# Kernel optimization log

Measured on AMD Instinct MI355X. Metric: run time of the kernel, lower is better.

Reference implementation:

```python
import jax, jax.numpy as jnp
import numpy as np

EPS = 1e-8

def setup_inputs() -> dict:
    key = jax.random.key(0)
    k1, k2 = jax.random.split(key)
    N, C, S = 2000000, 32, 8
    feats = jax.random.normal(k1, (N, C), dtype=jnp.float32)
    seg_ids = jnp.sort(jax.random.randint(k2, (N,), 0, S, dtype=jnp.int32))
    weight = jnp.ones((1, C), dtype=jnp.float32)
    bias = jnp.zeros((1, C), dtype=jnp.float32)
    return {"feats": feats, "seg_ids": seg_ids, "weight": weight, "bias": bias, "num_segments": S}

def reference(feats, seg_ids, weight, bias, num_segments):
    # Per-instance (segment) mean: GlobalPoolingForward with average=True
    counts = jax.ops.segment_sum(jnp.ones((feats.shape[0], 1), feats.dtype), seg_ids,
                                 num_segments=num_segments)  # [S,1]
    counts = jnp.maximum(counts, 1.0)
    mean = jax.ops.segment_sum(feats, seg_ids, num_segments=num_segments) / counts  # [S,C]
    # BroadcastForward ADDITION with -mean
    centered = feats - mean[seg_ids]  # [N,C]
    # Second global pooling: per-instance variance
    var = jax.ops.segment_sum(centered * centered, seg_ids, num_segments=num_segments) / counts  # [S,C]
    inv_std = jax.lax.rsqrt(var + EPS)  # [S,C]
    # BroadcastForward MULTIPLICATION with inv_std, then affine
    norm = centered * inv_std[seg_ids]
    return norm * weight + bias
```

## Files before the change

### kernel.cpp

```cpp
#include <hip/hip_runtime.h>
#include <math.h>


#define WS_SUM   0
#define WS_SUMSQ 2048
#define WS_CNT   4096
#define WS_SCALE 4352
#define WS_SHIFT 6400

typedef float f32x4 __attribute__((ext_vector_type(4)));

__global__ void zero_ws_kernel(float* __restrict__ ws) {
    int t = blockIdx.x * blockDim.x + threadIdx.x;
    if (t < 4352) ws[t] = 0.0f;
}

#define ACC4(A, Q, V)                                        \
    do {                                                     \
        (A).x += (V).x; (A).y += (V).y;                      \
        (A).z += (V).z; (A).w += (V).w;                      \
        (Q).x += (V).x * (V).x; (Q).y += (V).y * (V).y;      \
        (Q).z += (V).z * (V).z; (Q).w += (V).w * (V).w;      \
    } while (0)

#define ADD4(A, B)                                           \
    do {                                                     \
        (A).x += (B).x; (A).y += (B).y;                      \
        (A).z += (B).z; (A).w += (B).w;                      \
    } while (0)

__global__ __launch_bounds__(256) void reduce_kernel(
        const float4* __restrict__ feats4, const int* __restrict__ seg,
        float* __restrict__ ws, int N, int chunk) {
    __shared__ float4 s_sum[256];
    __shared__ float4 s_sq[256];
    __shared__ int    s_c[256];
    float* sum_g   = ws + WS_SUM;
    float* sumsq_g = ws + WS_SUMSQ;
    float* cnt_g   = ws + WS_CNT;

    int t  = threadIdx.x;
    int cg = t & 7;
    int rl = t >> 3;
    int bstart = blockIdx.x * chunk;
    if (bstart >= N) return;
    int bend = min(N, bstart + chunk);
    int rows = bend - bstart;

    int seg_first = seg[bstart];
    int seg_last  = seg[bend - 1];

    if (seg_first == seg_last) {
        float4 a0 = make_float4(0.f,0.f,0.f,0.f), a1 = a0, a2 = a0, a3 = a0;
        float4 q0 = a0, q1 = a0, q2 = a0, q3 = a0;
        const float4* p = feats4 + (size_t)(bstart + rl) * 8 + cg;
        int r = rl;
        for (; r + 224 < rows; r += 256) {
            float4 v0 = p[0 * 256];
            float4 v1 = p[1 * 256];
            float4 v2 = p[2 * 256];
            float4 v3 = p[3 * 256];
            float4 v4 = p[4 * 256];
            float4 v5 = p[5 * 256];
            float4 v6 = p[6 * 256];
            float4 v7 = p[7 * 256];
            ACC4(a0, q0, v0);
            ACC4(a1, q1, v1);
            ACC4(a2, q2, v2);
            ACC4(a3, q3, v3);
            ACC4(a0, q0, v4);
            ACC4(a1, q1, v5);
            ACC4(a2, q2, v6);
            ACC4(a3, q3, v7);
            p += 8 * 256;
        }
        for (; r < rows; r += 32) {
            float4 v = *p;
            ACC4(a0, q0, v);
            p += 256;
        }
        ADD4(a0, a1); ADD4(a2, a3); ADD4(a0, a2);
        ADD4(q0, q1); ADD4(q2, q3); ADD4(q0, q2);
        s_sum[t] = a0;
        s_sq[t]  = q0;
        __syncthreads();
        for (int off = 128; off >= 8; off >>= 1) {
            if (t < off) {
                float4 a = s_sum[t + off], b = s_sq[t + off];
                ADD4(s_sum[t], a);
                ADD4(s_sq[t], b);
            }
            __syncthreads();
        }
        if (t < 8) {
            float4 a = s_sum[t], b = s_sq[t];
            int base = seg_first * 32 + t * 4;
            atomicAdd(&sum_g[base + 0], a.x);
            atomicAdd(&sum_g[base + 1], a.y);
            atomicAdd(&sum_g[base + 2], a.z);
            atomicAdd(&sum_g[base + 3], a.w);
            atomicAdd(&sumsq_g[base + 0], b.x);
            atomicAdd(&sumsq_g[base + 1], b.y);
            atomicAdd(&sumsq_g[base + 2], b.z);
            atomicAdd(&sumsq_g[base + 3], b.w);
        }
        if (t == 0) atomicAdd(&cnt_g[seg_first], (float)rows);
        return;
    }

    for (int s = seg_first; s <= seg_last; ++s) {
        float4 acc  = make_float4(0.f, 0.f, 0.f, 0.f);
        float4 accq = make_float4(0.f, 0.f, 0.f, 0.f);
        int c = 0;
        for (int r = bstart + rl; r < bend; r += 32) {
            if (seg[r] == s) {
                float4 v = feats4[(size_t)r * 8 + cg];
                ACC4(acc, accq, v);
                c++;
            }
        }
        s_sum[t] = acc;
        s_sq[t]  = accq;
        s_c[t]   = (cg == 0) ? c : 0;
        __syncthreads();
        for (int off = 128; off >= 8; off >>= 1) {
            if (t < off) {
                float4 a = s_sum[t + off], b = s_sq[t + off];
                ADD4(s_sum[t], a);
                ADD4(s_sq[t], b);
                s_c[t] += s_c[t + off];
            }
            __syncthreads();
        }
        if (t < 8) {
            float4 a = s_sum[t], b = s_sq[t];
            int base = s * 32 + t * 4;
            atomicAdd(&sum_g[base + 0], a.x);
            atomicAdd(&sum_g[base + 1], a.y);
            atomicAdd(&sum_g[base + 2], a.z);
            atomicAdd(&sum_g[base + 3], a.w);
            atomicAdd(&sumsq_g[base + 0], b.x);
            atomicAdd(&sumsq_g[base + 1], b.y);
            atomicAdd(&sumsq_g[base + 2], b.z);
            atomicAdd(&sumsq_g[base + 3], b.w);
        }
        if (t == 0) {
            int ctot = s_c[0] + s_c[1] + s_c[2] + s_c[3]
                     + s_c[4] + s_c[5] + s_c[6] + s_c[7];
            atomicAdd(&cnt_g[s], (float)ctot);
        }
        __syncthreads();
    }
}

__global__ void stats_kernel(const float* __restrict__ w,
                             const float* __restrict__ b,
                             const int* __restrict__ nsp,
                             float* __restrict__ ws) {
    const float* sum_g   = ws + WS_SUM;
    const float* sumsq_g = ws + WS_SUMSQ;
    const float* cnt_g   = ws + WS_CNT;
    float* scale_g = ws + WS_SCALE;
    float* shift_g = ws + WS_SHIFT;

    int t  = threadIdx.x;
    int ns = *nsp;
    for (int i = t; i < ns * 32; i += blockDim.x) {
        int s = i >> 5, c = i & 31;
        float cnt  = fmaxf(cnt_g[s], 1.0f);
        float mean = sum_g[i] / cnt;
        float var  = fmaxf(sumsq_g[i] / cnt - mean * mean, 0.0f);
        float inv  = rsqrtf(var + 1e-8f);
        float sc   = inv * w[c];
        scale_g[i] = sc;
        shift_g[i] = b[c] - mean * sc;
    }
}

__global__ __launch_bounds__(256) void apply_kernel(
        const float* __restrict__ feats, const int* __restrict__ seg,
        const float* __restrict__ ws, float* __restrict__ out, int total4) {
    const f32x4* f4 = (const f32x4*)feats;
    f32x4*       o4 = (f32x4*)out;
    const f32x4* scale4 = (const f32x4*)(ws + WS_SCALE);
    const f32x4* shift4 = (const f32x4*)(ws + WS_SHIFT);
    int stride = gridDim.x * blockDim.x;
    for (int i = blockIdx.x * blockDim.x + threadIdx.x; i < total4; i += stride) {
        int row = i >> 3, cg = i & 7;
        int s = seg[row];
        f32x4 v  = __builtin_nontemporal_load(&f4[i]);
        f32x4 sc = scale4[s * 8 + cg];
        f32x4 sh = shift4[s * 8 + cg];
        f32x4 o;
        o.x = fmaf(v.x, sc.x, sh.x);
        o.y = fmaf(v.y, sc.y, sh.y);
        o.z = fmaf(v.z, sc.z, sh.z);
        o.w = fmaf(v.w, sc.w, sh.w);
        __builtin_nontemporal_store(o, &o4[i]);
    }
}

extern "C" void kernel_launch(void* const* d_in, const int* in_sizes, int n_in,
                              void* d_out, int out_size, void* d_ws, size_t ws_size,
                              hipStream_t stream) {
    const float* feats = (const float*)d_in[0];
    const int*   seg   = (const int*)d_in[1];
    const float* w     = (const float*)d_in[2];
    const float* b     = (const float*)d_in[3];
    const int*   nsp   = (const int*)d_in[4];
    float* out = (float*)d_out;
    float* ws  = (float*)d_ws;

    int N = in_sizes[1];
    int total4 = N * 8;

    const int NB = 2048;
    int chunk = (N + NB - 1) / NB;

    hipLaunchKernelGGL(zero_ws_kernel, dim3(17), dim3(256), 0, stream, ws);
    hipLaunchKernelGGL(reduce_kernel, dim3(NB), dim3(256), 0, stream,
                       (const float4*)feats, seg, ws, N, chunk);
    hipLaunchKernelGGL(stats_kernel, dim3(1), dim3(256), 0, stream,
                       w, b, nsp, ws);
    hipLaunchKernelGGL(apply_kernel, dim3(4096), dim3(256), 0, stream,
                       feats, seg, ws, out, total4);
}
```

Baseline: 174.6 us.

## Fuse reduce, stats and apply into one cooperative kernel with grid sync

Replaces the separate reduce, stats and apply launches with a single cooperative kernel of 512 blocks. Each block reduces its chunk, waits at a grid-wide sync, recomputes scale and shift into shared memory, then normalizes the same chunk it just read, so that chunk may still be in cache on the second read. This removes two launches and the separate apply pass over the whole array. The cost is a grid barrier and occupancy limits from cooperative launch. A fallback to the old three-kernel path runs if the cooperative launch fails.

```diff
diff --git a/kernel.cpp b/kernel.cpp
--- a/kernel.cpp
+++ b/kernel.cpp
@@ -1,18 +1,19 @@
 #include <hip/hip_runtime.h>
+#include <hip/hip_cooperative_groups.h>
 #include <math.h>
+
+namespace cg = cooperative_groups;
 
 
 #define WS_SUM   0
 #define WS_SUMSQ 2048
 #define WS_CNT   4096
-#define WS_SCALE 4352
-#define WS_SHIFT 6400
 
 typedef float f32x4 __attribute__((ext_vector_type(4)));
 
 __global__ void zero_ws_kernel(float* __restrict__ ws) {
     int t = blockIdx.x * blockDim.x + threadIdx.x;
-    if (t < 4352) ws[t] = 0.0f;
+    if (t < 4160) ws[t] = 0.0f;
 }
 
 #define ACC4(A, Q, V)                                        \
@@ -29,31 +30,17 @@
         (A).z += (B).z; (A).w += (B).w;                      \
     } while (0)
 
-__global__ __launch_bounds__(256) void reduce_kernel(
+__device__ __forceinline__ void reduce_chunk(
         const float4* __restrict__ feats4, const int* __restrict__ seg,
-        float* __restrict__ ws, int N, int chunk) {
-    __shared__ float4 s_sum[256];
-    __shared__ float4 s_sq[256];
-    __shared__ int    s_c[256];
-    float* sum_g   = ws + WS_SUM;
-    float* sumsq_g = ws + WS_SUMSQ;
-    float* cnt_g   = ws + WS_CNT;
-
-    int t  = threadIdx.x;
-    int cg = t & 7;
-    int rl = t >> 3;
-    int bstart = blockIdx.x * chunk;
-    if (bstart >= N) return;
-    int bend = min(N, bstart + chunk);
-    int rows = bend - bstart;
-
-    int seg_first = seg[bstart];
-    int seg_last  = seg[bend - 1];
-
+        float* __restrict__ sum_g, float* __restrict__ sumsq_g,
+        float* __restrict__ cnt_g,
+        float4* s_sum, float4* s_sq, int* s_c,
+        int t, int cg_i, int rl,
+        int bstart, int bend, int rows, int seg_first, int seg_last) {
     if (seg_first == seg_last) {
         float4 a0 = make_float4(0.f,0.f,0.f,0.f), a1 = a0, a2 = a0, a3 = a0;
         float4 q0 = a0, q1 = a0, q2 = a0, q3 = a0;
-        const float4* p = feats4 + (size_t)(bstart + rl) * 8 + cg;
+        const float4* p = feats4 + (size_t)(bstart + rl) * 8 + cg_i;
         int r = rl;
         for (; r + 224 < rows; r += 256) {
             float4 v0 = p[0 * 256];
@@ -86,71 +73,187 @@
         __syncthreads();
         for (int off = 128; off >= 8; off >>= 1) {
             if (t < off) {
-                float4 a = s_sum[t + off], b = s_sq[t + off];
+                float4 a = s_sum[t + off], bb = s_sq[t + off];
                 ADD4(s_sum[t], a);
-                ADD4(s_sq[t], b);
+                ADD4(s_sq[t], bb);
             }
             __syncthreads();
         }
         if (t < 8) {
-            float4 a = s_sum[t], b = s_sq[t];
+            float4 a = s_sum[t], bb = s_sq[t];
             int base = seg_first * 32 + t * 4;
             atomicAdd(&sum_g[base + 0], a.x);
             atomicAdd(&sum_g[base + 1], a.y);
             atomicAdd(&sum_g[base + 2], a.z);
             atomicAdd(&sum_g[base + 3], a.w);
-            atomicAdd(&sumsq_g[base + 0], b.x);
-            atomicAdd(&sumsq_g[base + 1], b.y);
-            atomicAdd(&sumsq_g[base + 2], b.z);
-            atomicAdd(&sumsq_g[base + 3], b.w);
+            atomicAdd(&sumsq_g[base + 0], bb.x);
+            atomicAdd(&sumsq_g[base + 1], bb.y);
+            atomicAdd(&sumsq_g[base + 2], bb.z);
+            atomicAdd(&sumsq_g[base + 3], bb.w);
         }
         if (t == 0) atomicAdd(&cnt_g[seg_first], (float)rows);
-        return;
-    }
-
-    for (int s = seg_first; s <= seg_last; ++s) {
-        float4 acc  = make_float4(0.f, 0.f, 0.f, 0.f);
-        float4 accq = make_float4(0.f, 0.f, 0.f, 0.f);
-        int c = 0;
-        for (int r = bstart + rl; r < bend; r += 32) {
-            if (seg[r] == s) {
-                float4 v = feats4[(size_t)r * 8 + cg];
-                ACC4(acc, accq, v);
-                c++;
-            }
-        }
-        s_sum[t] = acc;
-        s_sq[t]  = accq;
-        s_c[t]   = (cg == 0) ? c : 0;
-        __syncthreads();
-        for (int off = 128; off >= 8; off >>= 1) {
-            if (t < off) {
-                float4 a = s_sum[t + off], b = s_sq[t + off];
-                ADD4(s_sum[t], a);
-                ADD4(s_sq[t], b);
-                s_c[t] += s_c[t + off];
-            }
+    } else {
+        for (int s = seg_first; s <= seg_last; ++s) {
+            float4 acc  = make_float4(0.f, 0.f, 0.f, 0.f);
+            float4 accq = make_float4(0.f, 0.f, 0.f, 0.f);
+            int c = 0;
+            for (int r = bstart + rl; r < bend; r += 32) {
+                if (seg[r] == s) {
+                    float4 v = feats4[(size_t)r * 8 + cg_i];
+                    ACC4(acc, accq, v);
+                    c++;
+                }
+            }
+            s_sum[t] = acc;
+            s_sq[t]  = accq;
+            s_c[t]   = (cg_i == 0) ? c : 0;
             __syncthreads();
-        }
-        if (t < 8) {
-            float4 a = s_sum[t], b = s_sq[t];
-            int base = s * 32 + t * 4;
-            atomicAdd(&sum_g[base + 0], a.x);
-            atomicAdd(&sum_g[base + 1], a.y);
-            atomicAdd(&sum_g[base + 2], a.z);
-            atomicAdd(&sum_g[base + 3], a.w);
-            atomicAdd(&sumsq_g[base + 0], b.x);
-            atomicAdd(&sumsq_g[base + 1], b.y);
-            atomicAdd(&sumsq_g[base + 2], b.z);
-            atomicAdd(&sumsq_g[base + 3], b.w);
-        }
-        if (t == 0) {
-            int ctot = s_c[0] + s_c[1] + s_c[2] + s_c[3]
-                     + s_c[4] + s_c[5] + s_c[6] + s_c[7];
-            atomicAdd(&cnt_g[s], (float)ctot);
-        }
-        __syncthreads();
-    }
+            for (int off = 128; off >= 8; off >>= 1) {
+                if (t < off) {
+                    float4 a = s_sum[t + off], bb = s_sq[t + off];
+                    ADD4(s_sum[t], a);
+                    ADD4(s_sq[t], bb);
+                    s_c[t] += s_c[t + off];
+                }
+                __syncthreads();
+            }
+            if (t < 8) {
+                float4 a = s_sum[t], bb = s_sq[t];
+                int base = s * 32 + t * 4;
+                atomicAdd(&sum_g[base + 0], a.x);
+                atomicAdd(&sum_g[base + 1], a.y);
+                atomicAdd(&sum_g[base + 2], a.z);
+                atomicAdd(&sum_g[base + 3], a.w);
+                atomicAdd(&sumsq_g[base + 0], bb.x);
+                atomicAdd(&sumsq_g[base + 1], bb.y);
+                atomicAdd(&sumsq_g[base + 2], bb.z);
+                atomicAdd(&sumsq_g[base + 3], bb.w);
+            }
+            if (t == 0) {
+                int ctot = s_c[0] + s_c[1] + s_c[2] + s_c[3]
+                         + s_c[4] + s_c[5] + s_c[6] + s_c[7];
+                atomicAdd(&cnt_g[s], (float)ctot);
+            }
+            __syncthreads();
+        }
+    }
+}
+
+__global__ __launch_bounds__(256, 2) void fused_kernel(
+        const float4* __restrict__ feats4, const int* __restrict__ seg,
+        const float* __restrict__ w, const float* __restrict__ b,
+        const int* __restrict__ nsp, float* __restrict__ ws,
+        float* __restrict__ out, int N, int chunk) {
+    __shared__ float4 s_sum[256];
+    __shared__ float4 s_sq[256];
+    __shared__ int    s_c[256];
+    __shared__ float  s_scale[2048];
+    __shared__ float  s_shift[2048];
+
+    float* sum_g   = ws + WS_SUM;
+    float* sumsq_g = ws + WS_SUMSQ;
+    float* cnt_g   = ws + WS_CNT;
+
+    int t  = threadIdx.x;
+    int cg_i = t & 7;
+    int rl = t >> 3;
+    int bstart = blockIdx.x * chunk;
+    int bend   = min(N, bstart + chunk);
+    bool active = bstart < N;
+    int rows = active ? (bend - bstart) : 0;
+    int seg_first = 0, seg_last = 0;
+
+    if (active) {
+        seg_first = seg[bstart];
+        seg_last  = seg[bend - 1];
+        reduce_chunk(feats4, seg, sum_g, sumsq_g, cnt_g,
+                     s_sum, s_sq, s_c, t, cg_i, rl,
+                     bstart, bend, rows, seg_first, seg_last);
+    }
+
+    cg::this_grid().sync();
+
+    int ns = *nsp;
+    int tot = min(ns, 64) * 32;
+    for (int i = t; i < tot; i += 256) {
+        int c = i & 31;
+        int s = i >> 5;
+        float cnt  = fmaxf(cnt_g[s], 1.0f);
+        float mean = sum_g[i] / cnt;
+        float var  = fmaxf(sumsq_g[i] / cnt - mean * mean, 0.0f);
+        float inv  = rsqrtf(var + 1e-8f);
+        float sc   = inv * w[c];
+        s_scale[i] = sc;
+        s_shift[i] = b[c] - mean * sc;
+    }
+    __syncthreads();
+
+    if (active) {
+        const f32x4* sc4 = (const f32x4*)s_scale;
+        const f32x4* sh4 = (const f32x4*)s_shift;
+        const f32x4* f4  = (const f32x4*)feats4;
+        f32x4*       o4  = (f32x4*)out;
+
+        if (seg_first == seg_last) {
+            f32x4 sc = sc4[seg_first * 8 + cg_i];
+            f32x4 sh = sh4[seg_first * 8 + cg_i];
+            int r = rl;
+            size_t idx = (size_t)(bstart + rl) * 8 + cg_i;
+            for (; r + 96 < rows; r += 128, idx += 1024) {
+                f32x4 v0 = f4[idx +   0];
+                f32x4 v1 = f4[idx + 256];
+                f32x4 v2 = f4[idx + 512];
+                f32x4 v3 = f4[idx + 768];
+                f32x4 o0, o1, o2, o3;
+                o0.x = fmaf(v0.x, sc.x, sh.x); o0.y = fmaf(v0.y, sc.y, sh.y);
+                o0.z = fmaf(v0.z, sc.z, sh.z); o0.w = fmaf(v0.w, sc.w, sh.w);
+                o1.x = fmaf(v1.x, sc.x, sh.x); o1.y = fmaf(v1.y, sc.y, sh.y);
+                o1.z = fmaf(v1.z, sc.z, sh.z); o1.w = fmaf(v1.w, sc.w, sh.w);
+                o2.x = fmaf(v2.x, sc.x, sh.x); o2.y = fmaf(v2.y, sc.y, sh.y);
+                o2.z = fmaf(v2.z, sc.z, sh.z); o2.w = fmaf(v2.w, sc.w, sh.w);
+                o3.x = fmaf(v3.x, sc.x, sh.x); o3.y = fmaf(v3.y, sc.y, sh.y);
+                o3.z = fmaf(v3.z, sc.z, sh.z); o3.w = fmaf(v3.w, sc.w, sh.w);
+                __builtin_nontemporal_store(o0, &o4[idx +   0]);
+                __builtin_nontemporal_store(o1, &o4[idx + 256]);
+                __builtin_nontemporal_store(o2, &o4[idx + 512]);
+                __builtin_nontemporal_store(o3, &o4[idx + 768]);
+            }
+            for (; r < rows; r += 32, idx += 256) {
+                f32x4 v = f4[idx];
+                f32x4 o;
+                o.x = fmaf(v.x, sc.x, sh.x); o.y = fmaf(v.y, sc.y, sh.y);
+                o.z = fmaf(v.z, sc.z, sh.z); o.w = fmaf(v.w, sc.w, sh.w);
+                __builtin_nontemporal_store(o, &o4[idx]);
+            }
+        } else {
+            for (int r = bstart + rl; r < bend; r += 32) {
+                int s = seg[r];
+                size_t idx = (size_t)r * 8 + cg_i;
+                f32x4 v  = f4[idx];
+                f32x4 sc = sc4[s * 8 + cg_i];
+                f32x4 sh = sh4[s * 8 + cg_i];
+                f32x4 o;
+                o.x = fmaf(v.x, sc.x, sh.x); o.y = fmaf(v.y, sc.y, sh.y);
+                o.z = fmaf(v.z, sc.z, sh.z); o.w = fmaf(v.w, sc.w, sh.w);
+                __builtin_nontemporal_store(o, &o4[idx]);
+            }
+        }
+    }
+}
+
+__global__ __launch_bounds__(256) void reduce_kernel(
+        const float4* __restrict__ feats4, const int* __restrict__ seg,
+        float* __restrict__ ws, int N, int chunk) {
+    __shared__ float4 s_sum[256];
+    __shared__ float4 s_sq[256];
+    __shared__ int    s_c[256];
+    int t  = threadIdx.x;
+    int bstart = blockIdx.x * chunk;
+    if (bstart >= N) return;
+    int bend = min(N, bstart + chunk);
+    reduce_chunk(feats4, seg, ws + WS_SUM, ws + WS_SUMSQ, ws + WS_CNT,
+                 s_sum, s_sq, s_c, t, t & 7, t >> 3,
+                 bstart, bend, bend - bstart, seg[bstart], seg[bend - 1]);
 }
 
 __global__ void stats_kernel(const float* __restrict__ w,
@@ -160,9 +263,8 @@
     const float* sum_g   = ws + WS_SUM;
     const float* sumsq_g = ws + WS_SUMSQ;
     const float* cnt_g   = ws + WS_CNT;
-    float* scale_g = ws + WS_SCALE;
-    float* shift_g = ws + WS_SHIFT;
-
+    float* scale_g = ws + WS_CNT + 64;
+    float* shift_g = ws + WS_CNT + 64 + 2048;
     int t  = threadIdx.x;
     int ns = *nsp;
     for (int i = t; i < ns * 32; i += blockDim.x) {
@@ -182,20 +284,18 @@
         const float* __restrict__ ws, float* __restrict__ out, int total4) {
     const f32x4* f4 = (const f32x4*)feats;
     f32x4*       o4 = (f32x4*)out;
-    const f32x4* scale4 = (const f32x4*)(ws + WS_SCALE);
-    const f32x4* shift4 = (const f32x4*)(ws + WS_SHIFT);
+    const f32x4* scale4 = (const f32x4*)(ws + WS_CNT + 64);
+    const f32x4* shift4 = (const f32x4*)(ws + WS_CNT + 64 + 2048);
     int stride = gridDim.x * blockDim.x;
     for (int i = blockIdx.x * blockDim.x + threadIdx.x; i < total4; i += stride) {
         int row = i >> 3, cg = i & 7;
         int s = seg[row];
-        f32x4 v  = __builtin_nontemporal_load(&f4[i]);
+        f32x4 v  = f4[i];
         f32x4 sc = scale4[s * 8 + cg];
         f32x4 sh = shift4[s * 8 + cg];
         f32x4 o;
-        o.x = fmaf(v.x, sc.x, sh.x);
-        o.y = fmaf(v.y, sc.y, sh.y);
-        o.z = fmaf(v.z, sc.z, sh.z);
-        o.w = fmaf(v.w, sc.w, sh.w);
+        o.x = fmaf(v.x, sc.x, sh.x); o.y = fmaf(v.y, sc.y, sh.y);
+        o.z = fmaf(v.z, sc.z, sh.z); o.w = fmaf(v.w, sc.w, sh.w);
         __builtin_nontemporal_store(o, &o4[i]);
     }
 }
@@ -214,14 +314,24 @@
     int N = in_sizes[1];
     int total4 = N * 8;
 
-    const int NB = 2048;
+    hipLaunchKernelGGL(zero_ws_kernel, dim3(17), dim3(256), 0, stream, ws);
+
+    const int NB = 512;
     int chunk = (N + NB - 1) / NB;
-
-    hipLaunchKernelGGL(zero_ws_kernel, dim3(17), dim3(256), 0, stream, ws);
-    hipLaunchKernelGGL(reduce_kernel, dim3(NB), dim3(256), 0, stream,
-                       (const float4*)feats, seg, ws, N, chunk);
-    hipLaunchKernelGGL(stats_kernel, dim3(1), dim3(256), 0, stream,
-                       w, b, nsp, ws);
-    hipLaunchKernelGGL(apply_kernel, dim3(4096), dim3(256), 0, stream,
-                       feats, seg, ws, out, total4);
-}
+    const float4* feats4 = (const float4*)feats;
+    void* args[] = { (void*)&feats4, (void*)&seg, (void*)&w, (void*)&b,
+                     (void*)&nsp, (void*)&ws, (void*)&out, (void*)&N, (void*)&chunk };
+    hipError_t err = hipLaunchCooperativeKernel((void*)fused_kernel, dim3(NB),
+                                                dim3(256), args, 0, stream);
+    if (err != hipSuccess) {
+        (void)hipGetLastError();
+        const int NB2 = 2048;
+        int chunk2 = (N + NB2 - 1) / NB2;
+        hipLaunchKernelGGL(reduce_kernel, dim3(NB2), dim3(256), 0, stream,
+                           feats4, seg, ws, N, chunk2);
+        hipLaunchKernelGGL(stats_kernel, dim3(1), dim3(256), 0, stream,
+                           w, b, nsp, ws);
+        hipLaunchKernelGGL(apply_kernel, dim3(4096), dim3(256), 0, stream,
+                           feats, seg, ws, out, total4);
+    }
+}
```

After: 274.0 us. +57.0%, slower.
